# Optimization experiments

Hardware: AMD Instinct MI355X
Metric: run time of the kernel (lower is better)

Reference implementation:

```python
import jax, jax.numpy as jnp
import numpy as np

B, T, E = 2, 2048, 768
H = 12
HD = E // H          # 64
ROT = 32             # rotary dim (= head_dim // 2 in CLVP)
SCALE = HD ** -0.5


def rotate_half(x):
    # split last dim into (2, d/2), rotate second half by 90 deg
    x = x.reshape(*x.shape[:-1], 2, x.shape[-1] // 2)
    x1, x2 = x[..., 0, :], x[..., 1, :]
    return jnp.concatenate([-x2, x1], axis=-1)


def apply_rotary_pos_emb(state, freqs):
    # state: (B*H, T, HD); freqs: (1, T, ROT)
    pos_emb_len = freqs.shape[-1]
    s_l, s_r = state[..., :pos_emb_len], state[..., pos_emb_len:]
    f = freqs[:, :, -s_l.shape[-1]:]
    s_l = s_l * jnp.cos(f) + rotate_half(s_l) * jnp.sin(f)
    return jnp.concatenate([s_l, s_r], axis=-1)


def setup_inputs() -> dict:
    key = jax.random.key(0)
    ks = jax.random.split(key, 6)
    hidden_states = jax.random.normal(ks[0], (B, T, E), dtype=jnp.float32)
    rotary_pos_emb = jax.random.uniform(ks[1], (1, T, ROT), dtype=jnp.float32)
    Wq = jax.random.normal(ks[2], (E, E), dtype=jnp.float32) * 0.02
    Wk = jax.random.normal(ks[3], (E, E), dtype=jnp.float32) * 0.02
    Wv = jax.random.normal(ks[4], (E, E), dtype=jnp.float32) * 0.02
    Wo = jax.random.normal(ks[5], (E, E), dtype=jnp.float32) * 0.02
    bo = jnp.zeros((E,), dtype=jnp.float32)
    return {"hidden_states": hidden_states, "rotary_pos_emb": rotary_pos_emb,
            "Wq": Wq, "Wk": Wk, "Wv": Wv, "Wo": Wo, "bo": bo}


def _shape(x):
    # (B, T, E) -> (B*H, T, HD)
    return x.reshape(B, T, H, HD).transpose(0, 2, 1, 3).reshape(B * H, T, HD)


def reference(hidden_states, rotary_pos_emb, Wq, Wk, Wv, Wo, bo):
    # nn.Linear: x @ W.T
    q = _shape(hidden_states @ Wq.T * SCALE)
    k = _shape(hidden_states @ Wk.T)
    v = _shape(hidden_states @ Wv.T)

    q = apply_rotary_pos_emb(q, rotary_pos_emb)
    k = apply_rotary_pos_emb(k, rotary_pos_emb)
    v = apply_rotary_pos_emb(v, rotary_pos_emb)  # CLVP applies RoPE to V too

    attn = jax.nn.softmax(jnp.einsum('bqd,bkd->bqk', q, k), axis=-1)  # (B*H, T, T)
    out = jnp.einsum('bqk,bkd->bqd', attn, v)                          # (B*H, T, HD)
    out = out.reshape(B, H, T, HD).transpose(0, 2, 1, 3).reshape(B, T, E)
    return out @ Wo.T + bo
```

## Files before the change

kernel.cpp:

```cpp
#include <hip/hip_runtime.h>
#include <hip/hip_bf16.h>

typedef unsigned short ushort_t;
typedef __attribute__((ext_vector_type(8))) short short8;
typedef __attribute__((ext_vector_type(4))) float f32x4;

constexpr int B  = 2;
constexpr int T  = 2048;
constexpr int E  = 768;
constexpr int H  = 12;
constexpr int HD = 64;

__device__ __forceinline__ ushort_t f2bf(float x) {
  unsigned int u = __float_as_uint(x);
  u += 0x7fffu + ((u >> 16) & 1u);
  return (ushort_t)(u >> 16);
}

__device__ __forceinline__ unsigned int pack_bf2(float a, float b) {
  __hip_bfloat162 h = __float22bfloat162_rn(float2{a, b});
  return *(unsigned int*)&h;
}

__device__ __forceinline__ int swz(int row, int col) {
  return row * 64 + ((((col >> 3) ^ (row & 7)) << 3) | (col & 7));
}
__device__ __forceinline__ int swz32(int row, int col) {
  return row * 32 + ((((col >> 3) ^ (row & 3)) << 3) | (col & 7));
}

__global__ __launch_bounds__(256) void cvt_all(
    const float* __restrict__ X,  const float* __restrict__ Wq,
    const float* __restrict__ Wk, const float* __restrict__ Wv,
    const float* __restrict__ Wo, const float* __restrict__ rope,
    ushort_t* __restrict__ Xb,  ushort_t* __restrict__ Wqb,
    ushort_t* __restrict__ Wkb, ushort_t* __restrict__ Wvb,
    ushort_t* __restrict__ Wob, float* __restrict__ ct, float* __restrict__ st)
{
  constexpr int NX4 = (B * T * E) / 4;
  constexpr int NW4 = (E * E) / 4;
  constexpr int NC4 = NX4 + 4 * NW4;
  int i = blockIdx.x * 256 + threadIdx.x;
  if (i < NC4) {
    const float* s; ushort_t* d; int j;
    if (i < NX4) { s = X; d = Xb; j = i; }
    else {
      int t = i - NX4;
      int w = t / NW4; j = t - w * NW4;
      s = (w == 0) ? Wq : (w == 1) ? Wk : (w == 2) ? Wv : Wo;
      d = (w == 0) ? Wqb : (w == 1) ? Wkb : (w == 2) ? Wvb : Wob;
    }
    float4 v = ((const float4*)s)[j];
    ushort4 o;
    o.x = f2bf(v.x); o.y = f2bf(v.y); o.z = f2bf(v.z); o.w = f2bf(v.w);
    ((ushort4*)d)[j] = o;
  } else {
    int j = (i - NC4) * 4;
    float4 f = *(const float4*)(rope + j);
    float c, s;
    sincosf(f.x, &s, &c); ct[j+0] = c; st[j+0] = s;
    sincosf(f.y, &s, &c); ct[j+1] = c; st[j+1] = s;
    sincosf(f.z, &s, &c); ct[j+2] = c; st[j+2] = s;
    sincosf(f.w, &s, &c); ct[j+3] = c; st[j+3] = s;
  }
}

__global__ __launch_bounds__(256) void qkv_gemm(
    const ushort_t* __restrict__ Xb,
    const ushort_t* __restrict__ Wqb, const ushort_t* __restrict__ Wkb,
    const ushort_t* __restrict__ Wvb,
    const float* __restrict__ ct, const float* __restrict__ st,
    ushort_t* __restrict__ qfb, ushort_t* __restrict__ kfb, ushort_t* __restrict__ vfb)
{
  __shared__ __align__(16) ushort_t smem[64 * 132];
  ushort_t* Xs = smem;
  ushort_t* Ws = smem + 128 * 32;
  const int tid  = threadIdx.x;
  const int wave = tid >> 6;
  const int lane = tid & 63;
  const int l15  = lane & 15, quad = lane >> 4;
  const int n0 = blockIdx.x * 64;
  const int m0 = blockIdx.y * 128;
  const int z  = blockIdx.z;
  const ushort_t* Wt = (z == 0) ? Wqb : (z == 1) ? Wkb : Wvb;
  const int h = n0 >> 6;

  f32x4 acc[2][4];
  #pragma unroll
  for (int i = 0; i < 2; ++i)
    #pragma unroll
    for (int j = 0; j < 4; ++j) acc[i][j] = (f32x4){0.f, 0.f, 0.f, 0.f};

  const int srX = tid >> 1, scX = (tid & 1) * 16;
  const int srW = tid >> 2, scW = (tid & 3) * 8;

  for (int k0 = 0; k0 < E; k0 += 32) {
    uint4 xa = *(const uint4*)(Xb + (size_t)(m0 + srX) * E + k0 + scX);
    uint4 xc = *(const uint4*)(Xb + (size_t)(m0 + srX) * E + k0 + scX + 8);
    uint4 wa = *(const uint4*)(Wt + (size_t)(n0 + srW) * E + k0 + scW);
    *(uint4*)&Xs[swz32(srX, scX)]     = xa;
    *(uint4*)&Xs[swz32(srX, scX + 8)] = xc;
    *(uint4*)&Ws[swz32(srW, scW)]     = wa;
    __syncthreads();
    short8 a[2];
    #pragma unroll
    for (int mt = 0; mt < 2; ++mt)
      a[mt] = *(const short8*)&Xs[swz32(wave * 32 + mt * 16 + l15, quad * 8)];
    #pragma unroll
    for (int nt = 0; nt < 4; ++nt) {
      short8 bb = *(const short8*)&Ws[swz32(nt * 16 + l15, quad * 8)];
      #pragma unroll
      for (int mt = 0; mt < 2; ++mt)
        acc[mt][nt] = __builtin_amdgcn_mfma_f32_16x16x32_bf16(a[mt], bb, acc[mt][nt], 0, 0, 0);
    }
    __syncthreads();
  }

  const int b  = m0 >> 11;
  const int t0 = m0 & (T - 1);
  const int bh = b * H + h;
  const float qscale = (z == 0) ? 0.125f : 1.0f;

  if (z < 2) {
    #pragma unroll
    for (int mt = 0; mt < 2; ++mt) {
      #pragma unroll
      for (int r = 0; r < 4; ++r) {
        int mloc = wave * 32 + mt * 16 + quad * 4 + r;
        int t = (m0 + mloc) & (T - 1);
        float s0 = acc[mt][0][r] * qscale;
        float s1 = acc[mt][1][r] * qscale;
        float c0v = ct[t * 32 + l15],      sn0 = st[t * 32 + l15];
        float c1v = ct[t * 32 + 16 + l15], sn1 = st[t * 32 + 16 + l15];
        smem[swz(mloc, l15)]      = f2bf(s0 * c0v - s1 * sn0);
        smem[swz(mloc, 16 + l15)] = f2bf(s1 * c1v + s0 * sn1);
        smem[swz(mloc, 32 + l15)] = f2bf(acc[mt][2][r] * qscale);
        smem[swz(mloc, 48 + l15)] = f2bf(acc[mt][3][r] * qscale);
      }
    }
    __syncthreads();
    if (z == 0) {
      #pragma unroll
      for (int i = 0; i < 4; ++i) {
        int p = tid + 256 * i;
        int qtl = p >> 7, kh = (p >> 6) & 1, ln = p & 63;
        int tl = qtl * 16 + (ln & 15);
        int d  = kh * 32 + (ln >> 4) * 8;
        uint4 v = *(const uint4*)&smem[swz(tl, d)];
        size_t off = ((size_t)((bh * 128 + (t0 >> 4) + qtl) * 2 + kh)) * 512 + ln * 8;
        *(uint4*)(qfb + off) = v;
      }
    } else {
      #pragma unroll
      for (int i = 0; i < 4; ++i) {
        int p = tid + 256 * i;
        int ktl = p >> 9, mt = (p >> 7) & 3, kh = (p >> 6) & 1, ln = p & 63;
        int tl = ktl * 64 + mt * 16 + (ln & 15);
        int d  = kh * 32 + (ln >> 4) * 8;
        uint4 v = *(const uint4*)&smem[swz(tl, d)];
        size_t off = ((size_t)(((bh * 32 + (t0 >> 6) + ktl) * 4 + mt) * 2 + kh)) * 512 + ln * 8;
        *(uint4*)(kfb + off) = v;
      }
    }
  } else {
    #pragma unroll
    for (int mt = 0; mt < 2; ++mt) {
      #pragma unroll
      for (int r = 0; r < 4; ++r) {
        int mloc = wave * 32 + mt * 16 + quad * 4 + r;
        int t = (m0 + mloc) & (T - 1);
        float s0 = acc[mt][0][r], s1 = acc[mt][1][r];
        float c0v = ct[t * 32 + l15],      sn0 = st[t * 32 + l15];
        float c1v = ct[t * 32 + 16 + l15], sn1 = st[t * 32 + 16 + l15];
        smem[(l15)      * 132 + mloc] = f2bf(s0 * c0v - s1 * sn0);
        smem[(16 + l15) * 132 + mloc] = f2bf(s1 * c1v + s0 * sn1);
        smem[(32 + l15) * 132 + mloc] = f2bf(acc[mt][2][r]);
        smem[(48 + l15) * 132 + mloc] = f2bf(acc[mt][3][r]);
      }
    }
    __syncthreads();
    #pragma unroll
    for (int i = 0; i < 4; ++i) {
      int p = tid + 256 * i;
      int ktl = p >> 9, nt = (p >> 7) & 3, kh = (p >> 6) & 1, ln = p & 63;
      int d  = nt * 16 + (ln & 15);
      int tl = ktl * 64 + kh * 32 + (ln >> 4) * 8;
      uint4 v = *(const uint4*)&smem[d * 132 + tl];
      size_t off = ((size_t)(((bh * 32 + (t0 >> 6) + ktl) * 4 + nt) * 2 + kh)) * 512 + ln * 8;
      *(uint4*)(vfb + off) = v;
    }
  }
}

__global__ __launch_bounds__(256) void attn_kernel(
    const ushort_t* __restrict__ qfb, const ushort_t* __restrict__ kfb,
    const ushort_t* __restrict__ vfb, ushort_t* __restrict__ cbuf)
{
  __shared__ __align__(16) ushort_t Ps[4][16 * 64];
  const int tid  = threadIdx.x;
  const int wave = tid >> 6;
  const int lane = tid & 63;
  const int l15  = lane & 15, quad = lane >> 4;
  const int q0 = blockIdx.x * 64;
  const int bh = blockIdx.y;
  const ushort_t* Qf = qfb + (size_t)bh * (T * HD);
  const ushort_t* Kf = kfb + (size_t)bh * (T * HD);
  const ushort_t* Vf = vfb + (size_t)bh * (T * HD);
  ushort_t* Pw = &Ps[wave][0];

  short8 qa[2];
  #pragma unroll
  for (int kh = 0; kh < 2; ++kh)
    qa[kh] = *(const short8*)(Qf + ((size_t)(((q0 >> 4) + wave) * 2 + kh)) * 512 + lane * 8);

  short8 ka[4][2];
  #pragma unroll
  for (int mt = 0; mt < 4; ++mt)
    #pragma unroll
    for (int kh = 0; kh < 2; ++kh)
      ka[mt][kh] = *(const short8*)(Kf + ((size_t)(mt * 2 + kh)) * 512 + lane * 8);

  f32x4 o[4];
  #pragma unroll
  for (int nt = 0; nt < 4; ++nt) o[nt] = (f32x4){0.f, 0.f, 0.f, 0.f};
  float lsum = 0.f;

  for (int kt = 0; kt < T / 64; ++kt) {
    short8 va[4][2], kn[4][2];
    #pragma unroll
    for (int nt = 0; nt < 4; ++nt)
      #pragma unroll
      for (int kh = 0; kh < 2; ++kh)
        va[nt][kh] = *(const short8*)(Vf + ((size_t)((kt * 4 + nt) * 2 + kh)) * 512 + lane * 8);
    const int ktn = (kt + 1 < T / 64) ? kt + 1 : kt;
    #pragma unroll
    for (int mt = 0; mt < 4; ++mt)
      #pragma unroll
      for (int kh = 0; kh < 2; ++kh)
        kn[mt][kh] = *(const short8*)(Kf + ((size_t)((ktn * 4 + mt) * 2 + kh)) * 512 + lane * 8);

    f32x4 ss[4];
    #pragma unroll
    for (int mt = 0; mt < 4; ++mt) ss[mt] = (f32x4){0.f, 0.f, 0.f, 0.f};
    #pragma unroll
    for (int mt = 0; mt < 4; ++mt) {
      ss[mt] = __builtin_amdgcn_mfma_f32_16x16x32_bf16(ka[mt][0], qa[0], ss[mt], 0, 0, 0);
      ss[mt] = __builtin_amdgcn_mfma_f32_16x16x32_bf16(ka[mt][1], qa[1], ss[mt], 0, 0, 0);
    }

    #pragma unroll
    for (int mt = 0; mt < 4; ++mt) {
      float p0 = __expf(ss[mt][0]);
      float p1 = __expf(ss[mt][1]);
      float p2 = __expf(ss[mt][2]);
      float p3 = __expf(ss[mt][3]);
      lsum += (p0 + p1) + (p2 + p3);
      uint2 w2;
      w2.x = pack_bf2(p0, p1);
      w2.y = pack_bf2(p2, p3);
      *(uint2*)&Pw[swz(l15, mt * 16 + quad * 4)] = w2;
    }

    short8 pa0 = *(const short8*)&Pw[swz(l15, quad * 8)];
    short8 pa1 = *(const short8*)&Pw[swz(l15, 32 + quad * 8)];
    #pragma unroll
    for (int nt = 0; nt < 4; ++nt) {
      o[nt] = __builtin_amdgcn_mfma_f32_16x16x32_bf16(pa0, va[nt][0], o[nt], 0, 0, 0);
      o[nt] = __builtin_amdgcn_mfma_f32_16x16x32_bf16(pa1, va[nt][1], o[nt], 0, 0, 0);
    }

    #pragma unroll
    for (int mt = 0; mt < 4; ++mt) {
      ka[mt][0] = kn[mt][0];
      ka[mt][1] = kn[mt][1];
    }
  }

  lsum += __shfl_xor(lsum, 16);
  lsum += __shfl_xor(lsum, 32);

  const int b = bh / H, h = bh % H;
  #pragma unroll
  for (int r = 0; r < 4; ++r) {
    float lr = __shfl(lsum, quad * 4 + r);
    float inv = 1.0f / lr;
    int t = q0 + wave * 16 + quad * 4 + r;
    size_t base = ((size_t)b * T + t) * E + h * HD;
    cbuf[base + l15]      = f2bf(o[0][r] * inv);
    cbuf[base + 16 + l15] = f2bf(o[1][r] * inv);
    cbuf[base + 32 + l15] = f2bf(o[2][r] * inv);
    cbuf[base + 48 + l15] = f2bf(o[3][r] * inv);
  }
}

__global__ __launch_bounds__(256) void out_gemm(
    const ushort_t* __restrict__ Xc, const ushort_t* __restrict__ Wob,
    const float* __restrict__ bo, float* __restrict__ out)
{
  __shared__ __align__(16) ushort_t Xs[128][40];
  __shared__ __align__(16) ushort_t Ws[64][40];
  const int tid  = threadIdx.x;
  const int wave = tid >> 6;
  const int lane = tid & 63;
  const int l15  = lane & 15, quad = lane >> 4;
  const int n0 = blockIdx.x * 64;
  const int m0 = blockIdx.y * 128;

  f32x4 acc[2][4];
  #pragma unroll
  for (int i = 0; i < 2; ++i)
    #pragma unroll
    for (int j = 0; j < 4; ++j) acc[i][j] = (f32x4){0.f, 0.f, 0.f, 0.f};

  const int srX = tid >> 1, scX = (tid & 1) * 16;
  const int srW = tid >> 2, scW = (tid & 3) * 8;

  for (int k0 = 0; k0 < E; k0 += 32) {
    *(uint4*)&Xs[srX][scX]     = *(const uint4*)(Xc + (size_t)(m0 + srX) * E + k0 + scX);
    *(uint4*)&Xs[srX][scX + 8] = *(const uint4*)(Xc + (size_t)(m0 + srX) * E + k0 + scX + 8);
    *(uint4*)&Ws[srW][scW]     = *(const uint4*)(Wob + (size_t)(n0 + srW) * E + k0 + scW);
    __syncthreads();
    #pragma unroll
    for (int mt = 0; mt < 2; ++mt) {
      short8 a = *(const short8*)&Xs[wave * 32 + mt * 16 + l15][quad * 8];
      #pragma unroll
      for (int nt = 0; nt < 4; ++nt) {
        short8 bb = *(const short8*)&Ws[nt * 16 + l15][quad * 8];
        acc[mt][nt] = __builtin_amdgcn_mfma_f32_16x16x32_bf16(a, bb, acc[mt][nt], 0, 0, 0);
      }
    }
    __syncthreads();
  }

  float bias[4];
  #pragma unroll
  for (int nt = 0; nt < 4; ++nt) bias[nt] = bo[n0 + nt * 16 + l15];
  #pragma unroll
  for (int mt = 0; mt < 2; ++mt) {
    #pragma unroll
    for (int r = 0; r < 4; ++r) {
      int m = m0 + wave * 32 + mt * 16 + quad * 4 + r;
      float* op = out + (size_t)m * E + n0;
      op[l15]      = acc[mt][0][r] + bias[0];
      op[16 + l15] = acc[mt][1][r] + bias[1];
      op[32 + l15] = acc[mt][2][r] + bias[2];
      op[48 + l15] = acc[mt][3][r] + bias[3];
    }
  }
}

extern "C" void kernel_launch(void* const* d_in, const int* in_sizes, int n_in,
                              void* d_out, int out_size, void* d_ws, size_t ws_size,
                              hipStream_t stream) {
  (void)in_sizes; (void)n_in; (void)out_size; (void)ws_size;
  const float* X    = (const float*)d_in[0];
  const float* rope = (const float*)d_in[1];
  const float* Wq   = (const float*)d_in[2];
  const float* Wk   = (const float*)d_in[3];
  const float* Wv   = (const float*)d_in[4];
  const float* Wo   = (const float*)d_in[5];
  const float* bo   = (const float*)d_in[6];
  float* out = (float*)d_out;

  const size_t NX = (size_t)B * T * E;
  const size_t NW = (size_t)E * E;
  const size_t NR = (size_t)T * 32;
  ushort_t* Xb  = (ushort_t*)d_ws;
  ushort_t* Wqb = Xb  + NX;
  ushort_t* Wkb = Wqb + NW;
  ushort_t* Wvb = Wkb + NW;
  ushort_t* Wob = Wvb + NW;
  ushort_t* qfb = Wob + NW;
  ushort_t* kfb = qfb + NX;
  ushort_t* vfb = kfb + NX;
  ushort_t* cb  = vfb + NX;
  float* ct = (float*)(cb + NX);
  float* st = ct + NR;

  const int total4 = (int)((NX + 4 * NW + NR) / 4);
  cvt_all<<<total4 / 256, 256, 0, stream>>>(X, Wq, Wk, Wv, Wo, rope,
                                            Xb, Wqb, Wkb, Wvb, Wob, ct, st);

  qkv_gemm<<<dim3(E / 64, (B * T) / 128, 3), 256, 0, stream>>>(
      Xb, Wqb, Wkb, Wvb, ct, st, qfb, kfb, vfb);
  attn_kernel<<<dim3(T / 64, B * H), 256, 0, stream>>>(qfb, kfb, vfb, cb);
  out_gemm<<<dim3(E / 64, (B * T) / 128), 256, 0, stream>>>(cb, Wob, bo, out);
}
```

Measured before the change: 185.3 us.

## Split attention keys across waves per query tile; deepen GEMM k-step to 64

The attention kernel now gives each block only 16 queries and splits the key range across its four waves. Each wave loads K and V for its own key tiles, and the partial outputs and row sums are reduced through shared memory before one vectorized bf16 store. This launches four times as many blocks and sets a launch-bounds occupancy hint, at the cost of dropping the K register prefetch and adding an LDS reduction. Both GEMM kernels also move from a k-step of 32 to 64 with XOR-swizzled 64-wide tiles, which halves the number of barrier pairs.

```diff
diff --git a/kernel.cpp b/kernel.cpp
--- a/kernel.cpp
+++ b/kernel.cpp
@@ -24,9 +24,6 @@
 
 __device__ __forceinline__ int swz(int row, int col) {
   return row * 64 + ((((col >> 3) ^ (row & 7)) << 3) | (col & 7));
-}
-__device__ __forceinline__ int swz32(int row, int col) {
-  return row * 32 + ((((col >> 3) ^ (row & 3)) << 3) | (col & 7));
 }
 
 __global__ __launch_bounds__(256) void cvt_all(
@@ -72,9 +69,9 @@
     const float* __restrict__ ct, const float* __restrict__ st,
     ushort_t* __restrict__ qfb, ushort_t* __restrict__ kfb, ushort_t* __restrict__ vfb)
 {
-  __shared__ __align__(16) ushort_t smem[64 * 132];
+  __shared__ __align__(16) ushort_t smem[128 * 64 + 64 * 64];
   ushort_t* Xs = smem;
-  ushort_t* Ws = smem + 128 * 32;
+  ushort_t* Ws = smem + 128 * 64;
   const int tid  = threadIdx.x;
   const int wave = tid >> 6;
   const int lane = tid & 63;
@@ -91,27 +88,38 @@
     #pragma unroll
     for (int j = 0; j < 4; ++j) acc[i][j] = (f32x4){0.f, 0.f, 0.f, 0.f};
 
-  const int srX = tid >> 1, scX = (tid & 1) * 16;
-  const int srW = tid >> 2, scW = (tid & 3) * 8;
-
-  for (int k0 = 0; k0 < E; k0 += 32) {
-    uint4 xa = *(const uint4*)(Xb + (size_t)(m0 + srX) * E + k0 + scX);
-    uint4 xc = *(const uint4*)(Xb + (size_t)(m0 + srX) * E + k0 + scX + 8);
-    uint4 wa = *(const uint4*)(Wt + (size_t)(n0 + srW) * E + k0 + scW);
-    *(uint4*)&Xs[swz32(srX, scX)]     = xa;
-    *(uint4*)&Xs[swz32(srX, scX + 8)] = xc;
-    *(uint4*)&Ws[swz32(srW, scW)]     = wa;
-    __syncthreads();
-    short8 a[2];
+  const int srX = tid >> 1, scX = (tid & 1) * 32;
+  const int srW = tid >> 2, scW = (tid & 3) * 16;
+
+  for (int k0 = 0; k0 < E; k0 += 64) {
+    uint4 x0 = *(const uint4*)(Xb + (size_t)(m0 + srX) * E + k0 + scX);
+    uint4 x1 = *(const uint4*)(Xb + (size_t)(m0 + srX) * E + k0 + scX + 8);
+    uint4 x2 = *(const uint4*)(Xb + (size_t)(m0 + srX) * E + k0 + scX + 16);
+    uint4 x3 = *(const uint4*)(Xb + (size_t)(m0 + srX) * E + k0 + scX + 24);
+    uint4 w0 = *(const uint4*)(Wt + (size_t)(n0 + srW) * E + k0 + scW);
+    uint4 w1 = *(const uint4*)(Wt + (size_t)(n0 + srW) * E + k0 + scW + 8);
+    *(uint4*)&Xs[swz(srX, scX)]      = x0;
+    *(uint4*)&Xs[swz(srX, scX + 8)]  = x1;
+    *(uint4*)&Xs[swz(srX, scX + 16)] = x2;
+    *(uint4*)&Xs[swz(srX, scX + 24)] = x3;
+    *(uint4*)&Ws[swz(srW, scW)]      = w0;
+    *(uint4*)&Ws[swz(srW, scW + 8)]  = w1;
+    __syncthreads();
+    short8 a[2][2];
     #pragma unroll
     for (int mt = 0; mt < 2; ++mt)
-      a[mt] = *(const short8*)&Xs[swz32(wave * 32 + mt * 16 + l15, quad * 8)];
+      #pragma unroll
+      for (int kh = 0; kh < 2; ++kh)
+        a[mt][kh] = *(const short8*)&Xs[swz(wave * 32 + mt * 16 + l15, kh * 32 + quad * 8)];
     #pragma unroll
     for (int nt = 0; nt < 4; ++nt) {
-      short8 bb = *(const short8*)&Ws[swz32(nt * 16 + l15, quad * 8)];
-      #pragma unroll
-      for (int mt = 0; mt < 2; ++mt)
-        acc[mt][nt] = __builtin_amdgcn_mfma_f32_16x16x32_bf16(a[mt], bb, acc[mt][nt], 0, 0, 0);
+      #pragma unroll
+      for (int kh = 0; kh < 2; ++kh) {
+        short8 bb = *(const short8*)&Ws[swz(nt * 16 + l15, kh * 32 + quad * 8)];
+        #pragma unroll
+        for (int mt = 0; mt < 2; ++mt)
+          acc[mt][nt] = __builtin_amdgcn_mfma_f32_16x16x32_bf16(a[mt][kh], bb, acc[mt][nt], 0, 0, 0);
+      }
     }
     __syncthreads();
   }
@@ -192,16 +200,18 @@
   }
 }
 
-__global__ __launch_bounds__(256) void attn_kernel(
+__global__ __launch_bounds__(256, 5) void attn_kernel(
     const ushort_t* __restrict__ qfb, const ushort_t* __restrict__ kfb,
     const ushort_t* __restrict__ vfb, ushort_t* __restrict__ cbuf)
 {
   __shared__ __align__(16) ushort_t Ps[4][16 * 64];
+  __shared__ __align__(16) float Osh[4][16][68];
+  __shared__ float Lsh[4][16];
   const int tid  = threadIdx.x;
   const int wave = tid >> 6;
   const int lane = tid & 63;
   const int l15  = lane & 15, quad = lane >> 4;
-  const int q0 = blockIdx.x * 64;
+  const int qg = blockIdx.x;
   const int bh = blockIdx.y;
   const ushort_t* Qf = qfb + (size_t)bh * (T * HD);
   const ushort_t* Kf = kfb + (size_t)bh * (T * HD);
@@ -211,33 +221,22 @@
   short8 qa[2];
   #pragma unroll
   for (int kh = 0; kh < 2; ++kh)
-    qa[kh] = *(const short8*)(Qf + ((size_t)(((q0 >> 4) + wave) * 2 + kh)) * 512 + lane * 8);
-
-  short8 ka[4][2];
-  #pragma unroll
-  for (int mt = 0; mt < 4; ++mt)
-    #pragma unroll
-    for (int kh = 0; kh < 2; ++kh)
-      ka[mt][kh] = *(const short8*)(Kf + ((size_t)(mt * 2 + kh)) * 512 + lane * 8);
+    qa[kh] = *(const short8*)(Qf + ((size_t)(qg * 2 + kh)) * 512 + lane * 8);
 
   f32x4 o[4];
   #pragma unroll
   for (int nt = 0; nt < 4; ++nt) o[nt] = (f32x4){0.f, 0.f, 0.f, 0.f};
   float lsum = 0.f;
 
-  for (int kt = 0; kt < T / 64; ++kt) {
-    short8 va[4][2], kn[4][2];
-    #pragma unroll
-    for (int nt = 0; nt < 4; ++nt)
-      #pragma unroll
-      for (int kh = 0; kh < 2; ++kh)
-        va[nt][kh] = *(const short8*)(Vf + ((size_t)((kt * 4 + nt) * 2 + kh)) * 512 + lane * 8);
-    const int ktn = (kt + 1 < T / 64) ? kt + 1 : kt;
+  for (int kt = wave; kt < T / 64; kt += 4) {
+    short8 ka[4][2], va[4][2];
     #pragma unroll
     for (int mt = 0; mt < 4; ++mt)
       #pragma unroll
-      for (int kh = 0; kh < 2; ++kh)
-        kn[mt][kh] = *(const short8*)(Kf + ((size_t)((ktn * 4 + mt) * 2 + kh)) * 512 + lane * 8);
+      for (int kh = 0; kh < 2; ++kh) {
+        ka[mt][kh] = *(const short8*)(Kf + ((size_t)((kt * 4 + mt) * 2 + kh)) * 512 + lane * 8);
+        va[mt][kh] = *(const short8*)(Vf + ((size_t)((kt * 4 + mt) * 2 + kh)) * 512 + lane * 8);
+      }
 
     f32x4 ss[4];
     #pragma unroll
@@ -268,37 +267,43 @@
       o[nt] = __builtin_amdgcn_mfma_f32_16x16x32_bf16(pa0, va[nt][0], o[nt], 0, 0, 0);
       o[nt] = __builtin_amdgcn_mfma_f32_16x16x32_bf16(pa1, va[nt][1], o[nt], 0, 0, 0);
     }
-
-    #pragma unroll
-    for (int mt = 0; mt < 4; ++mt) {
-      ka[mt][0] = kn[mt][0];
-      ka[mt][1] = kn[mt][1];
-    }
   }
 
   lsum += __shfl_xor(lsum, 16);
   lsum += __shfl_xor(lsum, 32);
-
+  if (lane < 16) Lsh[wave][l15] = lsum;
+
+  #pragma unroll
+  for (int nt = 0; nt < 4; ++nt)
+    #pragma unroll
+    for (int r = 0; r < 4; ++r)
+      Osh[wave][quad * 4 + r][nt * 16 + l15] = o[nt][r];
+  __syncthreads();
+
+  const int row = tid >> 4;
+  const int c4  = (tid & 15) * 4;
+  float4 s = *(const float4*)&Osh[0][row][c4];
+  #pragma unroll
+  for (int w = 1; w < 4; ++w) {
+    float4 t = *(const float4*)&Osh[w][row][c4];
+    s.x += t.x; s.y += t.y; s.z += t.z; s.w += t.w;
+  }
+  float inv = 1.0f / (Lsh[0][row] + Lsh[1][row] + Lsh[2][row] + Lsh[3][row]);
   const int b = bh / H, h = bh % H;
-  #pragma unroll
-  for (int r = 0; r < 4; ++r) {
-    float lr = __shfl(lsum, quad * 4 + r);
-    float inv = 1.0f / lr;
-    int t = q0 + wave * 16 + quad * 4 + r;
-    size_t base = ((size_t)b * T + t) * E + h * HD;
-    cbuf[base + l15]      = f2bf(o[0][r] * inv);
-    cbuf[base + 16 + l15] = f2bf(o[1][r] * inv);
-    cbuf[base + 32 + l15] = f2bf(o[2][r] * inv);
-    cbuf[base + 48 + l15] = f2bf(o[3][r] * inv);
-  }
+  int t = qg * 16 + row;
+  size_t base = ((size_t)b * T + t) * E + h * HD + c4;
+  uint2 w2;
+  w2.x = pack_bf2(s.x * inv, s.y * inv);
+  w2.y = pack_bf2(s.z * inv, s.w * inv);
+  *(uint2*)(cbuf + base) = w2;
 }
 
 __global__ __launch_bounds__(256) void out_gemm(
     const ushort_t* __restrict__ Xc, const ushort_t* __restrict__ Wob,
     const float* __restrict__ bo, float* __restrict__ out)
 {
-  __shared__ __align__(16) ushort_t Xs[128][40];
-  __shared__ __align__(16) ushort_t Ws[64][40];
+  __shared__ __align__(16) ushort_t Xs[128 * 64];
+  __shared__ __align__(16) ushort_t Ws[64 * 64];
   const int tid  = threadIdx.x;
   const int wave = tid >> 6;
   const int lane = tid & 63;
@@ -312,21 +317,37 @@
     #pragma unroll
     for (int j = 0; j < 4; ++j) acc[i][j] = (f32x4){0.f, 0.f, 0.f, 0.f};
 
-  const int srX = tid >> 1, scX = (tid & 1) * 16;
-  const int srW = tid >> 2, scW = (tid & 3) * 8;
-
-  for (int k0 = 0; k0 < E; k0 += 32) {
-    *(uint4*)&Xs[srX][scX]     = *(const uint4*)(Xc + (size_t)(m0 + srX) * E + k0 + scX);
-    *(uint4*)&Xs[srX][scX + 8] = *(const uint4*)(Xc + (size_t)(m0 + srX) * E + k0 + scX + 8);
-    *(uint4*)&Ws[srW][scW]     = *(const uint4*)(Wob + (size_t)(n0 + srW) * E + k0 + scW);
-    __syncthreads();
-    #pragma unroll
-    for (int mt = 0; mt < 2; ++mt) {
-      short8 a = *(const short8*)&Xs[wave * 32 + mt * 16 + l15][quad * 8];
-      #pragma unroll
-      for (int nt = 0; nt < 4; ++nt) {
-        short8 bb = *(const short8*)&Ws[nt * 16 + l15][quad * 8];
-        acc[mt][nt] = __builtin_amdgcn_mfma_f32_16x16x32_bf16(a, bb, acc[mt][nt], 0, 0, 0);
+  const int srX = tid >> 1, scX = (tid & 1) * 32;
+  const int srW = tid >> 2, scW = (tid & 3) * 16;
+
+  for (int k0 = 0; k0 < E; k0 += 64) {
+    uint4 x0 = *(const uint4*)(Xc + (size_t)(m0 + srX) * E + k0 + scX);
+    uint4 x1 = *(const uint4*)(Xc + (size_t)(m0 + srX) * E + k0 + scX + 8);
+    uint4 x2 = *(const uint4*)(Xc + (size_t)(m0 + srX) * E + k0 + scX + 16);
+    uint4 x3 = *(const uint4*)(Xc + (size_t)(m0 + srX) * E + k0 + scX + 24);
+    uint4 w0 = *(const uint4*)(Wob + (size_t)(n0 + srW) * E + k0 + scW);
+    uint4 w1 = *(const uint4*)(Wob + (size_t)(n0 + srW) * E + k0 + scW + 8);
+    *(uint4*)&Xs[swz(srX, scX)]      = x0;
+    *(uint4*)&Xs[swz(srX, scX + 8)]  = x1;
+    *(uint4*)&Xs[swz(srX, scX + 16)] = x2;
+    *(uint4*)&Xs[swz(srX, scX + 24)] = x3;
+    *(uint4*)&Ws[swz(srW, scW)]      = w0;
+    *(uint4*)&Ws[swz(srW, scW + 8)]  = w1;
+    __syncthreads();
+    short8 a[2][2];
+    #pragma unroll
+    for (int mt = 0; mt < 2; ++mt)
+      #pragma unroll
+      for (int kh = 0; kh < 2; ++kh)
+        a[mt][kh] = *(const short8*)&Xs[swz(wave * 32 + mt * 16 + l15, kh * 32 + quad * 8)];
+    #pragma unroll
+    for (int nt = 0; nt < 4; ++nt) {
+      #pragma unroll
+      for (int kh = 0; kh < 2; ++kh) {
+        short8 bb = *(const short8*)&Ws[swz(nt * 16 + l15, kh * 32 + quad * 8)];
+        #pragma unroll
+        for (int mt = 0; mt < 2; ++mt)
+          acc[mt][nt] = __builtin_amdgcn_mfma_f32_16x16x32_bf16(a[mt][kh], bb, acc[mt][nt], 0, 0, 0);
       }
     }
     __syncthreads();
@@ -383,6 +404,6 @@
 
   qkv_gemm<<<dim3(E / 64, (B * T) / 128, 3), 256, 0, stream>>>(
       Xb, Wqb, Wkb, Wvb, ct, st, qfb, kfb, vfb);
-  attn_kernel<<<dim3(T / 64, B * H), 256, 0, stream>>>(qfb, kfb, vfb, cb);
+  attn_kernel<<<dim3(T / 16, B * H), 256, 0, stream>>>(qfb, kfb, vfb, cb);
   out_gemm<<<dim3(E / 64, (B * T) / 128), 256, 0, stream>>>(cb, Wob, bo, out);
 }
```

Measured after the change: 185.5 us. About the same (+0.1%).
